# Optimization experiments

Measured on AMD Instinct MI355X. Metric: run time of the kernel, lower is better.

Reference implementation:

```python
import jax, jax.numpy as jnp
import numpy as np

CF_ITERS = 5
CF_K = 0.02
DECAY = [0.9, 0.93, 0.85, 0.97, 0.88, 0.94]
N_CHAMBERS = 6
RES_DIM = 100
B = 262144

COUPLING = np.array([
    [0.0, -0.3, 0.6, 0.4, -0.2, 0.3],
    [-0.3, 0.0, -0.5, -0.7, 0.6, 0.4],
    [0.6, -0.5, 0.0, 0.3, -0.3, 0.2],
    [0.4, -0.7, 0.3, 0.0, -0.4, 0.5],
    [-0.2, 0.6, -0.3, -0.4, 0.0, 0.3],
    [0.3, 0.4, 0.2, 0.5, 0.3, 0.0]], dtype=np.float32)


def _init_linear(key, c, fan_out, fan_in):
    kw, kb = jax.random.split(key)
    bound = 1.0 / np.sqrt(fan_in)
    W = jax.random.uniform(kw, (c, fan_out, fan_in), jnp.float32, -bound, bound)
    b = jax.random.uniform(kb, (c, fan_out), jnp.float32, -bound, bound)
    return W, b


def setup_inputs() -> dict:
    key = jax.random.key(0)
    ks = jax.random.split(key, 5)
    res = jax.random.normal(ks[0], (B, RES_DIM), jnp.float32)
    W1, b1 = _init_linear(ks[1], N_CHAMBERS, 128, RES_DIM)
    W2, b2 = _init_linear(ks[2], N_CHAMBERS, 64, 128)
    W3, b3 = _init_linear(ks[3], N_CHAMBERS, 32, 64)
    W4, b4 = _init_linear(ks[4], N_CHAMBERS, 1, 32)
    coupling = jnp.asarray(COUPLING)
    return {"res": res, "W1": W1, "b1": b1, "W2": W2, "b2": b2,
            "W3": W3, "b3": b3, "W4": W4, "b4": b4, "coupling": coupling}


def reference(res, W1, b1, W2, b2, W3, b3, W4, b4, coupling):
    silu = jax.nn.silu
    # batched 6 per-chamber MLPs: [B, C, hidden]
    h = silu(jnp.einsum('bd,chd->bch', res, W1) + b1)      # [B,6,128]
    h = silu(jnp.einsum('bch,coh->bco', h, W2) + b2)       # [B,6,64]
    h = silu(jnp.einsum('bco,cpo->bcp', h, W3) + b3)       # [B,6,32]
    raw = (jnp.einsum('bcp,cqp->bcq', h, W4) + b4)[..., 0]  # [B,6]
    act = jax.nn.sigmoid(raw)
    decay = jnp.asarray(DECAY, dtype=jnp.float32)
    for _ in range(CF_ITERS):
        act = act * decay
        # infl[b,i,j] = CF_K * sin(act[b,j] - act[b,i])
        infl = CF_K * jnp.sin(act[:, None, :] - act[:, :, None])  # [B,6,6]
        act = act + jnp.sum(infl * coupling[None], axis=2)
        act = jnp.clip(act, 0.0, 1.0)
    return (act, raw)
```

## Files before the change

kernel.cpp:

```cpp
#include <hip/hip_runtime.h>


typedef unsigned int u32;
typedef __attribute__((ext_vector_type(8))) short bf16x8;
typedef __attribute__((ext_vector_type(4))) float f32x4;

#define RES_DIM 100
#define NCH 6
#define FRAGS_PER_CH 52
#define NFRAG (NCH*FRAGS_PER_CH)
#define WS_BYTES ((size_t)NFRAG*2048)

#define MFMA16 __builtin_amdgcn_mfma_f32_16x16x32_bf16

union FragU { bf16x8 v; u32 u[4]; uint4 q; };

__device__ __forceinline__ void split2(float f0, float f1, u32 &hp, u32 &lp){
    u32 h;
    asm("v_cvt_pk_bf16_f32 %0, %1, %2" : "=v"(h) : "v"(f0), "v"(f1));
    float l0 = f0 - __uint_as_float(h << 16);
    float l1 = f1 - __uint_as_float(h & 0xffff0000u);
    u32 l;
    asm("v_cvt_pk_bf16_f32 %0, %1, %2" : "=v"(l) : "v"(l0), "v"(l1));
    hp = h; lp = l;
}

__device__ __forceinline__ float silu1(float x){
    return x * __builtin_amdgcn_rcpf(1.f + __expf(-x));
}
__device__ __forceinline__ f32x4 silu4(f32x4 v){
    f32x4 r; r[0]=silu1(v[0]); r[1]=silu1(v[1]); r[2]=silu1(v[2]); r[3]=silu1(v[3]); return r;
}
__device__ __forceinline__ float sin_rev(float x){ return __builtin_amdgcn_sinf(x*0.15915494309189535f); }

__device__ __forceinline__ void load_frag(const u32* __restrict__ wsb, int frag, int lane,
                                          bf16x8 &h, bf16x8 &l){
    const uint4* p = (const uint4*)(wsb + ((size_t)frag << 9) + (lane << 3));
    FragU H, L; H.q = p[0]; L.q = p[1];
    h = H.v; l = L.v;
}

__device__ __forceinline__ f32x4 triple(f32x4 acc, bf16x8 ah, bf16x8 al, bf16x8 bh, bf16x8 bl){
    acc = MFMA16(ah, bh, acc, 0, 0, 0);
    acc = MFMA16(al, bh, acc, 0, 0, 0);
    acc = MFMA16(ah, bl, acc, 0, 0, 0);
    return acc;
}

__global__ void __launch_bounds__(256) prep_kernel(
    const float* __restrict__ W1, const float* __restrict__ W2,
    const float* __restrict__ W3, u32* __restrict__ ws)
{
    const int f = blockIdx.x * 4 + (threadIdx.x >> 6);
    const int lane = threadIdx.x & 63;
    const int c = f / FRAGS_PER_CH, r = f % FRAGS_PER_CH;
    const int n15 = lane & 15, quad = lane >> 4;
    float vals[8];
    if (r < 32) {
        int n = r >> 2, k = r & 3;
        const float* wp = W1 + (size_t)c*128*RES_DIM + (size_t)(n*16 + n15)*RES_DIM;
        #pragma unroll
        for (int j=0;j<8;j++){
            int kk = k*32 + quad*8 + j;
            vals[j] = (kk < RES_DIM) ? wp[kk] : 0.f;
        }
    } else if (r < 48) {
        int rr = r - 32; int n = rr >> 2, k = rr & 3;
        const float* wp = W2 + (size_t)c*64*128 + (size_t)(n*16 + n15)*128;
        #pragma unroll
        for (int j=0;j<8;j++) vals[j] = wp[k*32 + quad*8 + j];
    } else {
        int rr = r - 48; int n = rr >> 1, k = rr & 1;
        const float* wp = W3 + (size_t)c*32*64 + (size_t)(n*16 + n15)*64;
        #pragma unroll
        for (int j=0;j<8;j++) vals[j] = wp[k*32 + quad*8 + j];
    }
    u32 hp[4], lp[4];
    #pragma unroll
    for (int i=0;i<4;i++) split2(vals[2*i], vals[2*i+1], hp[i], lp[i]);
    u32* dst = ws + ((size_t)f << 9) + (lane << 3);
    *(uint4*)(dst)     = make_uint4(hp[0],hp[1],hp[2],hp[3]);
    *(uint4*)(dst + 4) = make_uint4(lp[0],lp[1],lp[2],lp[3]);
}

#define TB_STRIDE 36
#define TB_SIZE (32*TB_STRIDE)

__global__ void __launch_bounds__(256, 2) chambers_mfma(
    const float* __restrict__ res, const u32* __restrict__ wsb,
    const float* __restrict__ b1, const float* __restrict__ b2,
    const float* __restrict__ b3, const float* __restrict__ W4,
    const float* __restrict__ b4, const float* __restrict__ Cpl,
    float* __restrict__ out, int nsamp)
{
    __shared__ __align__(16) float tb[4][TB_SIZE];
    __shared__ float rawld[4*32*7];

    const int tid  = threadIdx.x;
    const int w    = tid >> 6, lane = tid & 63;
    const int n15  = lane & 15, quad = lane >> 4;
    const int m_base = (blockIdx.x * 4 + w) * 32;

    bf16x8 rh[2][4], rl[2][4];
    #pragma unroll
    for (int mt=0; mt<2; mt++){
        const float* row = res + (size_t)(m_base + mt*16 + n15) * RES_DIM;
        #pragma unroll
        for (int ks=0; ks<4; ks++){
            float v[8];
            if (ks < 3){
                float4 A = *(const float4*)(row + ks*32 + quad*8);
                float4 B = *(const float4*)(row + ks*32 + quad*8 + 4);
                v[0]=A.x; v[1]=A.y; v[2]=A.z; v[3]=A.w;
                v[4]=B.x; v[5]=B.y; v[6]=B.z; v[7]=B.w;
            } else {
                float4 A = make_float4(0.f,0.f,0.f,0.f);
                if (quad == 0) A = *(const float4*)(row + 96);
                v[0]=A.x; v[1]=A.y; v[2]=A.z; v[3]=A.w;
                v[4]=0.f; v[5]=0.f; v[6]=0.f; v[7]=0.f;
            }
            FragU H, L;
            #pragma unroll
            for (int i=0;i<4;i++) split2(v[2*i], v[2*i+1], H.u[i], L.u[i]);
            rh[mt][ks]=H.v; rl[mt][ks]=L.v;
        }
    }

    for (int c=0; c<NCH; c++){
        const float* b1c = b1 + c*128;
        const float* b2c = b2 + c*64;
        const float* b3c = b3 + c*32;
        const int fbase = c*FRAGS_PER_CH;

        f32x4 c2[2][4];
        #pragma unroll
        for (int mt=0; mt<2; mt++)
            #pragma unroll
            for (int nt=0; nt<4; nt++){
                float bb = b2c[nt*16 + n15];
                f32x4 t = {bb,bb,bb,bb}; c2[mt][nt] = t;
            }

        for (int kk=0; kk<4; kk++){
            bf16x8 w2h[4], w2l[4];
            #pragma unroll
            for (int nt=0; nt<4; nt++) load_frag(wsb, fbase + 32 + nt*4 + kk, lane, w2h[nt], w2l[nt]);

            #pragma unroll
            for (int pp=0; pp<2; pp++){
                int p = kk*2 + pp;
                float bb = b1c[p*16 + n15];
                f32x4 z = {0.f,0.f,0.f,0.f};
                f32x4 A0h = {bb,bb,bb,bb}, A0u = z, A0v = z;
                f32x4 A1h = A0h,           A1u = z, A1v = z;
                #pragma unroll
                for (int ks=0; ks<4; ks++){
                    bf16x8 bh, bl; load_frag(wsb, fbase + p*4 + ks, lane, bh, bl);
                    A0h = MFMA16(rh[0][ks], bh, A0h, 0,0,0);
                    A1h = MFMA16(rh[1][ks], bh, A1h, 0,0,0);
                    A0u = MFMA16(rl[0][ks], bh, A0u, 0,0,0);
                    A1u = MFMA16(rl[1][ks], bh, A1u, 0,0,0);
                    A0v = MFMA16(rh[0][ks], bl, A0v, 0,0,0);
                    A1v = MFMA16(rh[1][ks], bl, A1v, 0,0,0);
                }
                f32x4 s0 = silu4((A0h + A0u) + A0v);
                f32x4 s1 = silu4((A1h + A1u) + A1v);
                #pragma unroll
                for (int r=0; r<4; r++){
                    tb[w][(quad*4 + r)*TB_STRIDE      + pp*16 + n15] = s0[r];
                    tb[w][(16 + quad*4 + r)*TB_STRIDE + pp*16 + n15] = s1[r];
                }
            }
            __threadfence_block();
            bf16x8 a2h[2], a2l[2];
            #pragma unroll
            for (int mt=0; mt<2; mt++){
                const float* qp = &tb[w][(mt*16 + n15)*TB_STRIDE + quad*8];
                float4 A = *(const float4*)qp;
                float4 B = *(const float4*)(qp + 4);
                FragU H, L;
                split2(A.x, A.y, H.u[0], L.u[0]);
                split2(A.z, A.w, H.u[1], L.u[1]);
                split2(B.x, B.y, H.u[2], L.u[2]);
                split2(B.z, B.w, H.u[3], L.u[3]);
                a2h[mt]=H.v; a2l[mt]=L.v;
            }
            __threadfence_block();
            #pragma unroll
            for (int nt=0; nt<4; nt++){
                c2[0][nt] = triple(c2[0][nt], a2h[0], a2l[0], w2h[nt], w2l[nt]);
                c2[1][nt] = triple(c2[1][nt], a2h[1], a2l[1], w2h[nt], w2l[nt]);
            }
        }
        #pragma unroll
        for (int mt=0; mt<2; mt++)
            #pragma unroll
            for (int nt=0; nt<4; nt++) c2[mt][nt] = silu4(c2[mt][nt]);

        f32x4 c3[2][2];
        #pragma unroll
        for (int mt=0; mt<2; mt++)
            #pragma unroll
            for (int nt=0; nt<2; nt++){
                float bb = b3c[nt*16 + n15];
                f32x4 t = {bb,bb,bb,bb}; c3[mt][nt] = t;
            }
        for (int k3=0; k3<2; k3++){
            bf16x8 w3h[2], w3l[2];
            #pragma unroll
            for (int nt=0; nt<2; nt++) load_frag(wsb, fbase + 48 + nt*2 + k3, lane, w3h[nt], w3l[nt]);
            #pragma unroll
            for (int mt=0; mt<2; mt++)
                #pragma unroll
                for (int q2=0; q2<2; q2++)
                    #pragma unroll
                    for (int r=0; r<4; r++)
                        tb[w][(mt*16 + quad*4 + r)*TB_STRIDE + q2*16 + n15] = c2[mt][2*k3+q2][r];
            __threadfence_block();
            bf16x8 a3h[2], a3l[2];
            #pragma unroll
            for (int mt=0; mt<2; mt++){
                const float* qp = &tb[w][(mt*16 + n15)*TB_STRIDE + quad*8];
                float4 A = *(const float4*)qp;
                float4 B = *(const float4*)(qp + 4);
                FragU H, L;
                split2(A.x, A.y, H.u[0], L.u[0]);
                split2(A.z, A.w, H.u[1], L.u[1]);
                split2(B.x, B.y, H.u[2], L.u[2]);
                split2(B.z, B.w, H.u[3], L.u[3]);
                a3h[mt]=H.v; a3l[mt]=L.v;
            }
            __threadfence_block();
            #pragma unroll
            for (int nt=0; nt<2; nt++){
                c3[0][nt] = triple(c3[0][nt], a3h[0], a3l[0], w3h[nt], w3l[nt]);
                c3[1][nt] = triple(c3[1][nt], a3h[1], a3l[1], w3h[nt], w3l[nt]);
            }
        }
        #pragma unroll
        for (int mt=0; mt<2; mt++)
            #pragma unroll
            for (int nt=0; nt<2; nt++) c3[mt][nt] = silu4(c3[mt][nt]);

        float w4a = W4[c*32 + n15];
        float w4b = W4[c*32 + 16 + n15];
        float bb4 = b4[c];
        #pragma unroll
        for (int mt=0; mt<2; mt++){
            float t0 = c3[mt][0][0]*w4a + c3[mt][1][0]*w4b;
            float t1 = c3[mt][0][1]*w4a + c3[mt][1][1]*w4b;
            float t2 = c3[mt][0][2]*w4a + c3[mt][1][2]*w4b;
            float t3 = c3[mt][0][3]*w4a + c3[mt][1][3]*w4b;
            #pragma unroll
            for (int off=1; off<16; off<<=1){
                t0 += __shfl_xor(t0, off, 64);
                t1 += __shfl_xor(t1, off, 64);
                t2 += __shfl_xor(t2, off, 64);
                t3 += __shfl_xor(t3, off, 64);
            }
            if (n15 == 0){
                int mb = w*32 + mt*16 + quad*4;
                rawld[(mb+0)*7 + c] = t0 + bb4;
                rawld[(mb+1)*7 + c] = t1 + bb4;
                rawld[(mb+2)*7 + c] = t2 + bb4;
                rawld[(mb+3)*7 + c] = t3 + bb4;
            }
        }
    }
    __threadfence_block();

    const int m = lane & 31;
    float rw[6], a[6];
    #pragma unroll
    for (int j=0;j<6;j++){
        rw[j] = rawld[(w*32 + m)*7 + j];
        a[j]  = __builtin_amdgcn_rcpf(1.f + __expf(-rw[j]));
    }
    const float dec[6] = {0.9f,0.93f,0.85f,0.97f,0.88f,0.94f};
    float C[6][6];
    #pragma unroll
    for (int i=0;i<6;i++)
        #pragma unroll
        for (int j=0;j<6;j++) C[i][j] = Cpl[i*6+j];
    #pragma unroll
    for (int it=0; it<5; it++){
        #pragma unroll
        for (int j=0;j<6;j++) a[j] *= dec[j];
        float nz[6];
        #pragma unroll
        for (int i=0;i<6;i++){
            float sum = 0.f;
            #pragma unroll
            for (int j=0;j<6;j++) sum += sin_rev(a[j]-a[i]) * C[i][j];
            nz[i] = a[i] + 0.02f*sum;
        }
        #pragma unroll
        for (int i=0;i<6;i++) a[i] = fminf(fmaxf(nz[i],0.f),1.f);
    }
    if (lane < 32){
        size_t s = (size_t)m_base + m;
        #pragma unroll
        for (int j=0;j<6;j++) out[s*6 + j] = a[j];
        size_t rb = (size_t)nsamp*6 + s*6;
        #pragma unroll
        for (int j=0;j<6;j++) out[rb + j] = rw[j];
    }
}

__global__ void __launch_bounds__(256, 2) chambers_fb(
    const float* __restrict__ res, const float* __restrict__ W1, const float* __restrict__ b1,
    const float* __restrict__ W2, const float* __restrict__ b2,
    const float* __restrict__ W3, const float* __restrict__ b3,
    const float* __restrict__ W4, const float* __restrict__ b4,
    const float* __restrict__ Cpl, float* __restrict__ out, int nsamp)
{
    __shared__ float w2t[128*64];
    __shared__ float h3buf[256][33];
    __shared__ float rawbuf[256][7];
    const int tid = threadIdx.x;
    const long long s = (long long)blockIdx.x * 256 + tid;
    float rf[RES_DIM];
    {
        const float4* rp = (const float4*)(res + s*RES_DIM);
        #pragma unroll
        for (int i=0;i<25;i++){
            float4 v = rp[i];
            rf[4*i+0]=v.x; rf[4*i+1]=v.y; rf[4*i+2]=v.z; rf[4*i+3]=v.w;
        }
    }
    for (int c=0;c<6;c++){
        __syncthreads();
        {
            const float* w2c = W2 + c*64*128;
            for (int k=tid; k<64*128; k+=256){
                int o = k >> 7, u = k & 127;
                w2t[u*64 + o] = w2c[k];
            }
        }
        __syncthreads();
        const float* w1c = W1 + c*128*RES_DIM;
        const float* b1c = b1 + c*128;
        const float* b2c = b2 + c*64;
        float h2a[64];
        #pragma unroll
        for (int o=0;o<64;o++) h2a[o] = b2c[o];
        for (int u=0; u<128; u+=2){
            const float4* wa = (const float4*)(w1c + u*RES_DIM);
            const float4* wb = wa + 25;
            float a0=0.f,a1=0.f,a2=0.f,a3=0.f;
            #pragma unroll
            for (int i=0;i<25;i++){
                float4 va=wa[i], vb=wb[i];
                a0 = fmaf(va.x, rf[4*i+0], a0); a0 = fmaf(va.y, rf[4*i+1], a0);
                a2 = fmaf(va.z, rf[4*i+2], a2); a2 = fmaf(va.w, rf[4*i+3], a2);
                a1 = fmaf(vb.x, rf[4*i+0], a1); a1 = fmaf(vb.y, rf[4*i+1], a1);
                a3 = fmaf(vb.z, rf[4*i+2], a3); a3 = fmaf(vb.w, rf[4*i+3], a3);
            }
            float hh0 = silu1(a0+a2+b1c[u]);
            float hh1 = silu1(a1+a3+b1c[u+1]);
            const float* wr0 = &w2t[u*64];
            const float* wr1 = &w2t[(u+1)*64];
            #pragma unroll
            for (int o=0;o<64;o+=4){
                float4 va = *(const float4*)(wr0+o);
                float4 vb = *(const float4*)(wr1+o);
                h2a[o+0] = fmaf(va.x, hh0, fmaf(vb.x, hh1, h2a[o+0]));
                h2a[o+1] = fmaf(va.y, hh0, fmaf(vb.y, hh1, h2a[o+1]));
                h2a[o+2] = fmaf(va.z, hh0, fmaf(vb.z, hh1, h2a[o+2]));
                h2a[o+3] = fmaf(va.w, hh0, fmaf(vb.w, hh1, h2a[o+3]));
            }
        }
        #pragma unroll
        for (int o=0;o<64;o++) h2a[o] = silu1(h2a[o]);
        {
            const float* w3c = W3 + c*32*64;
            const float* b3c = b3 + c*32;
            for (int p=0; p<32; p+=2){
                const float4* wa = (const float4*)(w3c + p*64);
                const float4* wb = wa + 16;
                float a0=0.f,a1=0.f,a2=0.f,a3=0.f;
                #pragma unroll
                for (int k=0;k<16;k++){
                    float4 va=wa[k], vb=wb[k];
                    a0 = fmaf(va.x, h2a[4*k+0], a0); a0 = fmaf(va.y, h2a[4*k+1], a0);
                    a2 = fmaf(va.z, h2a[4*k+2], a2); a2 = fmaf(va.w, h2a[4*k+3], a2);
                    a1 = fmaf(vb.x, h2a[4*k+0], a1); a1 = fmaf(vb.y, h2a[4*k+1], a1);
                    a3 = fmaf(vb.z, h2a[4*k+2], a3); a3 = fmaf(vb.w, h2a[4*k+3], a3);
                }
                h3buf[tid][p]   = silu1(a0+a2+b3c[p]);
                h3buf[tid][p+1] = silu1(a1+a3+b3c[p+1]);
            }
        }
        {
            const float4* w4p = (const float4*)(W4 + c*32);
            float a0=0.f, a1=0.f;
            #pragma unroll
            for (int k=0;k<8;k++){
                float4 v = w4p[k];
                a0 = fmaf(v.x, h3buf[tid][4*k+0], a0);
                a1 = fmaf(v.y, h3buf[tid][4*k+1], a1);
                a0 = fmaf(v.z, h3buf[tid][4*k+2], a0);
                a1 = fmaf(v.w, h3buf[tid][4*k+3], a1);
            }
            rawbuf[tid][c] = a0+a1+b4[c];
        }
    }
    float a[6], rw[6];
    #pragma unroll
    for (int j=0;j<6;j++){ rw[j]=rawbuf[tid][j]; a[j]=__builtin_amdgcn_rcpf(1.f+__expf(-rw[j])); }
    const float dec[6] = {0.9f,0.93f,0.85f,0.97f,0.88f,0.94f};
    float C[6][6];
    #pragma unroll
    for (int i=0;i<6;i++)
        #pragma unroll
        for (int j=0;j<6;j++) C[i][j]=Cpl[i*6+j];
    #pragma unroll
    for (int it=0; it<5; it++){
        #pragma unroll
        for (int j=0;j<6;j++) a[j]*=dec[j];
        float nz[6];
        #pragma unroll
        for (int i=0;i<6;i++){
            float sum=0.f;
            #pragma unroll
            for (int j=0;j<6;j++) sum += sin_rev(a[j]-a[i]) * C[i][j];
            nz[i]=a[i]+0.02f*sum;
        }
        #pragma unroll
        for (int i=0;i<6;i++) a[i]=fminf(fmaxf(nz[i],0.f),1.f);
    }
    long long ob = s*6;
    #pragma unroll
    for (int j=0;j<6;j++) out[ob+j] = a[j];
    long long rb = (long long)nsamp*6 + ob;
    #pragma unroll
    for (int j=0;j<6;j++) out[rb+j] = rw[j];
}

extern "C" void kernel_launch(void* const* d_in, const int* in_sizes, int n_in,
                              void* d_out, int out_size, void* d_ws, size_t ws_size,
                              hipStream_t stream) {
    const float* res = (const float*)d_in[0];
    const float* W1  = (const float*)d_in[1];
    const float* b1  = (const float*)d_in[2];
    const float* W2  = (const float*)d_in[3];
    const float* b2  = (const float*)d_in[4];
    const float* W3  = (const float*)d_in[5];
    const float* b3  = (const float*)d_in[6];
    const float* W4  = (const float*)d_in[7];
    const float* b4  = (const float*)d_in[8];
    const float* Cpl = (const float*)d_in[9];
    float* out = (float*)d_out;
    int nsamp = in_sizes[0] / RES_DIM;

    if (ws_size >= WS_BYTES) {
        u32* ws = (u32*)d_ws;
        prep_kernel<<<NFRAG/4, 256, 0, stream>>>(W1, W2, W3, ws);
        chambers_mfma<<<nsamp/128, 256, 0, stream>>>(res, ws, b1, b2, b3, W4, b4, Cpl, out, nsamp);
    } else {
        chambers_fb<<<nsamp/256, 256, 0, stream>>>(res, W1, b1, W2, b2, W3, b3, W4, b4, Cpl, out, nsamp);
    }
}
```

Before: 429.5 us.

## Double-buffer layer-1 LDS staging to overlap layer-2 MFMAs with layer-1 compute

Gives the per-wave LDS tile two buffers, so layer 1 writes chunk kk into one buffer while layer 2 consumes chunk kk-1 from the other, with the last chunk drained after the loop. Layer 3 now writes both k-chunks at once and preloads all its weight fragments, removing two fences per chunk. The goal is to expose more independent MFMA work and hide LDS and fence latency. In exchange, LDS use per block doubles and register pressure rises, which could threaten the 2-blocks-per-SIMD occupancy target.

```diff
diff --git a/kernel.cpp b/kernel.cpp
--- a/kernel.cpp
+++ b/kernel.cpp
@@ -93,7 +93,7 @@
     const float* __restrict__ b4, const float* __restrict__ Cpl,
     float* __restrict__ out, int nsamp)
 {
-    __shared__ __align__(16) float tb[4][TB_SIZE];
+    __shared__ __align__(16) float tb[4][2][TB_SIZE];
     __shared__ float rawld[4*32*7];
 
     const int tid  = threadIdx.x;
@@ -141,11 +141,41 @@
                 f32x4 t = {bb,bb,bb,bb}; c2[mt][nt] = t;
             }
 
+        bf16x8 w2h[4], w2l[4];
+        float4 pA[2], pB[2];
+
+#define CONSUME_L2() do { \
+        bf16x8 a2h_[2], a2l_[2]; \
+        _Pragma("unroll") \
+        for (int mt=0; mt<2; mt++){ \
+            FragU H, L; \
+            split2(pA[mt].x, pA[mt].y, H.u[0], L.u[0]); \
+            split2(pA[mt].z, pA[mt].w, H.u[1], L.u[1]); \
+            split2(pB[mt].x, pB[mt].y, H.u[2], L.u[2]); \
+            split2(pB[mt].z, pB[mt].w, H.u[3], L.u[3]); \
+            a2h_[mt]=H.v; a2l_[mt]=L.v; \
+        } \
+        _Pragma("unroll") \
+        for (int nt=0; nt<4; nt++){ \
+            c2[0][nt] = triple(c2[0][nt], a2h_[0], a2l_[0], w2h[nt], w2l[nt]); \
+            c2[1][nt] = triple(c2[1][nt], a2h_[1], a2l_[1], w2h[nt], w2l[nt]); \
+        } \
+    } while(0)
+
         for (int kk=0; kk<4; kk++){
-            bf16x8 w2h[4], w2l[4];
-            #pragma unroll
-            for (int nt=0; nt<4; nt++) load_frag(wsb, fbase + 32 + nt*4 + kk, lane, w2h[nt], w2l[nt]);
-
+            float* tbw = &tb[w][kk & 1][0];
+            const float* tbr = &tb[w][(kk & 1) ^ 1][0];
+            if (kk > 0){
+                #pragma unroll
+                for (int mt=0; mt<2; mt++){
+                    const float* qp = tbr + (mt*16 + n15)*TB_STRIDE + quad*8;
+                    pA[mt] = *(const float4*)qp;
+                    pB[mt] = *(const float4*)(qp + 4);
+                }
+                #pragma unroll
+                for (int nt=0; nt<4; nt++)
+                    load_frag(wsb, fbase + 32 + nt*4 + (kk-1), lane, w2h[nt], w2l[nt]);
+            }
             #pragma unroll
             for (int pp=0; pp<2; pp++){
                 int p = kk*2 + pp;
@@ -167,35 +197,39 @@
                 f32x4 s1 = silu4((A1h + A1u) + A1v);
                 #pragma unroll
                 for (int r=0; r<4; r++){
-                    tb[w][(quad*4 + r)*TB_STRIDE      + pp*16 + n15] = s0[r];
-                    tb[w][(16 + quad*4 + r)*TB_STRIDE + pp*16 + n15] = s1[r];
+                    tbw[(quad*4 + r)*TB_STRIDE      + pp*16 + n15] = s0[r];
+                    tbw[(16 + quad*4 + r)*TB_STRIDE + pp*16 + n15] = s1[r];
                 }
             }
+            if (kk > 0) CONSUME_L2();
             __threadfence_block();
-            bf16x8 a2h[2], a2l[2];
+        }
+        {
+            const float* tbr = &tb[w][1][0];
             #pragma unroll
             for (int mt=0; mt<2; mt++){
-                const float* qp = &tb[w][(mt*16 + n15)*TB_STRIDE + quad*8];
-                float4 A = *(const float4*)qp;
-                float4 B = *(const float4*)(qp + 4);
-                FragU H, L;
-                split2(A.x, A.y, H.u[0], L.u[0]);
-                split2(A.z, A.w, H.u[1], L.u[1]);
-                split2(B.x, B.y, H.u[2], L.u[2]);
-                split2(B.z, B.w, H.u[3], L.u[3]);
-                a2h[mt]=H.v; a2l[mt]=L.v;
-            }
-            __threadfence_block();
-            #pragma unroll
-            for (int nt=0; nt<4; nt++){
-                c2[0][nt] = triple(c2[0][nt], a2h[0], a2l[0], w2h[nt], w2l[nt]);
-                c2[1][nt] = triple(c2[1][nt], a2h[1], a2l[1], w2h[nt], w2l[nt]);
-            }
-        }
+                const float* qp = tbr + (mt*16 + n15)*TB_STRIDE + quad*8;
+                pA[mt] = *(const float4*)qp;
+                pB[mt] = *(const float4*)(qp + 4);
+            }
+            #pragma unroll
+            for (int nt=0; nt<4; nt++)
+                load_frag(wsb, fbase + 32 + nt*4 + 3, lane, w2h[nt], w2l[nt]);
+            CONSUME_L2();
+        }
+#undef CONSUME_L2
+
         #pragma unroll
         for (int mt=0; mt<2; mt++)
             #pragma unroll
             for (int nt=0; nt<4; nt++) c2[mt][nt] = silu4(c2[mt][nt]);
+
+        bf16x8 w3h[2][2], w3l[2][2];
+        #pragma unroll
+        for (int k3=0; k3<2; k3++)
+            #pragma unroll
+            for (int nt=0; nt<2; nt++)
+                load_frag(wsb, fbase + 48 + nt*2 + k3, lane, w3h[k3][nt], w3l[k3][nt]);
 
         f32x4 c3[2][2];
         #pragma unroll
@@ -205,38 +239,44 @@
                 float bb = b3c[nt*16 + n15];
                 f32x4 t = {bb,bb,bb,bb}; c3[mt][nt] = t;
             }
-        for (int k3=0; k3<2; k3++){
-            bf16x8 w3h[2], w3l[2];
-            #pragma unroll
-            for (int nt=0; nt<2; nt++) load_frag(wsb, fbase + 48 + nt*2 + k3, lane, w3h[nt], w3l[nt]);
+        #pragma unroll
+        for (int k3=0; k3<2; k3++)
             #pragma unroll
             for (int mt=0; mt<2; mt++)
                 #pragma unroll
                 for (int q2=0; q2<2; q2++)
                     #pragma unroll
                     for (int r=0; r<4; r++)
-                        tb[w][(mt*16 + quad*4 + r)*TB_STRIDE + q2*16 + n15] = c2[mt][2*k3+q2][r];
-            __threadfence_block();
+                        tb[w][k3][(mt*16 + quad*4 + r)*TB_STRIDE + q2*16 + n15] = c2[mt][2*k3+q2][r];
+        __threadfence_block();
+        float4 qA[2][2], qB[2][2];
+        #pragma unroll
+        for (int k3=0; k3<2; k3++)
+            #pragma unroll
+            for (int mt=0; mt<2; mt++){
+                const float* qp = &tb[w][k3][(mt*16 + n15)*TB_STRIDE + quad*8];
+                qA[k3][mt] = *(const float4*)qp;
+                qB[k3][mt] = *(const float4*)(qp + 4);
+            }
+        #pragma unroll
+        for (int k3=0; k3<2; k3++){
             bf16x8 a3h[2], a3l[2];
             #pragma unroll
             for (int mt=0; mt<2; mt++){
-                const float* qp = &tb[w][(mt*16 + n15)*TB_STRIDE + quad*8];
-                float4 A = *(const float4*)qp;
-                float4 B = *(const float4*)(qp + 4);
                 FragU H, L;
-                split2(A.x, A.y, H.u[0], L.u[0]);
-                split2(A.z, A.w, H.u[1], L.u[1]);
-                split2(B.x, B.y, H.u[2], L.u[2]);
-                split2(B.z, B.w, H.u[3], L.u[3]);
+                split2(qA[k3][mt].x, qA[k3][mt].y, H.u[0], L.u[0]);
+                split2(qA[k3][mt].z, qA[k3][mt].w, H.u[1], L.u[1]);
+                split2(qB[k3][mt].x, qB[k3][mt].y, H.u[2], L.u[2]);
+                split2(qB[k3][mt].z, qB[k3][mt].w, H.u[3], L.u[3]);
                 a3h[mt]=H.v; a3l[mt]=L.v;
             }
-            __threadfence_block();
             #pragma unroll
             for (int nt=0; nt<2; nt++){
-                c3[0][nt] = triple(c3[0][nt], a3h[0], a3l[0], w3h[nt], w3l[nt]);
-                c3[1][nt] = triple(c3[1][nt], a3h[1], a3l[1], w3h[nt], w3l[nt]);
-            }
-        }
+                c3[0][nt] = triple(c3[0][nt], a3h[0], a3l[0], w3h[k3][nt], w3l[k3][nt]);
+                c3[1][nt] = triple(c3[1][nt], a3h[1], a3l[1], w3h[k3][nt], w3l[k3][nt]);
+            }
+        }
+        __threadfence_block();
         #pragma unroll
         for (int mt=0; mt<2; mt++)
             #pragma unroll
```

Result: slower. 448.2 us (+4.3%).
